# Kernel tuning notes

Hardware: AMD Instinct MI355X
Metric: run time of the kernel (lower is better)

## Reference

```python
import jax, jax.numpy as jnp
import numpy as np

B_IMG, T_PER, DIN = 8, 4096, 1176
D, E, BN, L, TOP_K, OUT = 1024, 8, 64, 4, 2, 4096


def setup_inputs() -> dict:
    key = jax.random.key(0)
    ks = jax.random.split(key, 16)
    s = 0.02
    inp = {
        "pixel_values": jax.random.normal(ks[0], (B_IMG * T_PER, DIN), jnp.float32),
        "image_grid_thw": jnp.tile(jnp.array([[1, 64, 64]], dtype=jnp.int64), (B_IMG, 1)),
        # in_proj (no bias)
        "w_in": jax.random.normal(ks[1], (DIN, D), jnp.float32) * s,
        # skin classifier: Linear(D,64) -> ReLU -> Linear(64,3)
        "w_sc1": jax.random.normal(ks[2], (D, 64), jnp.float32) * s,
        "b_sc1": jnp.zeros((64,), jnp.float32),
        "w_sc2": jax.random.normal(ks[3], (64, 3), jnp.float32) * s,
        "b_sc2": jnp.zeros((3,), jnp.float32),
        # per-adapter-layer routers (stacked over L)
        "w_rimg": jax.random.normal(ks[4], (L, D, E), jnp.float32) * s,
        "w_rskin": jax.random.normal(ks[5], (L, 3, E), jnp.float32) * s,
        # per-layer, per-expert MLP: Linear(D,BN) -> ReLU -> Linear(BN,D)
        "ew1": jax.random.normal(ks[6], (L, E, D, BN), jnp.float32) * s,
        "eb1": jnp.zeros((L, E, BN), jnp.float32),
        "ew2": jax.random.normal(ks[7], (L, E, BN, D), jnp.float32) * s,
        "eb2": jnp.zeros((L, E, D), jnp.float32),
        # out_proj
        "w_out": jax.random.normal(ks[8], (D, OUT), jnp.float32) * s,
        "b_out": jnp.zeros((OUT,), jnp.float32),
    }
    return inp


def _forward(pixel_values, image_grid_thw, w_in, w_sc1, b_sc1, w_sc2, b_sc2,
             w_rimg, w_rskin, ew1, eb1, ew2, eb2, w_out, b_out):
    B = image_grid_thw.shape[0]
    T = pixel_values.shape[0] // B  # equal chunk sizes (t*h*w identical per image)
    x = pixel_values.reshape(B, T, -1)

    def per_image(xc):  # xc: [T, din]
        h = xc @ w_in  # [T, D]
        g = h.mean(0)
        skin_logits = jax.nn.relu(g @ w_sc1 + b_sc1) @ w_sc2 + b_sc2  # [3]
        skin_probs = jax.nn.softmax(skin_logits)

        def layer(carry, params):
            h, aux = carry
            wri, wrs, W1, B1, W2, B2 = params
            logits = h @ wri + skin_probs @ wrs  # [T, E]
            probs = jax.nn.softmax(logits, axis=-1)
            tp, ti = jax.lax.top_k(probs, TOP_K)
            tp = tp / (tp.sum(-1, keepdims=True) + 1e-6)
            rows = jnp.arange(h.shape[0])[:, None]
            # dense per-token expert weights (0 for non-selected experts)
            wfull = jnp.zeros_like(probs).at[rows, ti].add(tp)
            mask = jnp.zeros_like(probs).at[rows, ti].add(1.0)
            h1 = jax.nn.relu(jnp.einsum('td,edb->teb', h, W1) + B1)  # [T,E,BN]
            h2 = jnp.einsum('teb,ebd->ted', h1, W2) + B2             # [T,E,D]
            moe_out = jnp.einsum('ted,te->td', h2, wfull)
            aux = aux + (probs.mean(0) * mask.mean(0)).sum() * probs.shape[-1]
            return (h + moe_out, aux), None

        (h, aux), _ = jax.lax.scan(layer, (h, jnp.zeros((), h.dtype)),
                                   (w_rimg, w_rskin, ew1, eb1, ew2, eb2))
        return h.mean(0), skin_logits, aux

    pooled, skin_logits, aux = jax.vmap(per_image)(x)
    vision_proj = pooled @ w_out + b_out
    return pooled, vision_proj, aux.sum(), skin_logits


def reference(pixel_values, image_grid_thw, w_in, w_sc1, b_sc1, w_sc2, b_sc2,
              w_rimg, w_rskin, ew1, eb1, ew2, eb2, w_out, b_out):
    return _forward(pixel_values, image_grid_thw, w_in, w_sc1, b_sc1, w_sc2, b_sc2,
                    w_rimg, w_rskin, ew1, eb1, ew2, eb2, w_out, b_out)
```

## Files before the change

kernel.cpp:

```cpp
#include <hip/hip_runtime.h>
#include <math.h>

#define TPI  4096
#define TT   32768
#define DIN  1176
#define KP   1184
#define DM   1024
#define NE   8
#define BN   64
#define NL   4
#define DOUT 4096

typedef __attribute__((ext_vector_type(4))) float floatx4;
typedef __attribute__((ext_vector_type(8))) short bf16x8;
typedef unsigned int uint;

__device__ inline short f2bf(float x) {
    unsigned u = __float_as_uint(x);
    u += 0x7fffu + ((u >> 16) & 1u);
    return (short)(u >> 16);
}
__device__ inline float bf2f(short h) {
    return __uint_as_float(((unsigned)(unsigned short)h) << 16);
}

#define GLP(p) ((const __attribute__((address_space(1))) void*)(p))
#define LDSP(p) ((__attribute__((address_space(3))) void*)(p))
#define ASYNC16(g, s) __builtin_amdgcn_global_load_lds(GLP(g), LDSP(s), 16, 0, 0)

#define OFF_H0    0ul
#define OFF_H1    67108864ul
#define OFF_XB    134217728ul
#define OFF_WBT   211812352ul
#define OFF_E1T   214237184ul
#define OFF_E2T   218431488ul
#define OFF_BTOK  222625792ul
#define OFF_BW1   222756864ul
#define OFF_BW2   222887936ul
#define OFF_T2E   223019008ul
#define OFF_T2W   223150080ul
#define OFF_WQ    223412224ul
#define OFF_Z     223416320ul
#define Z_BYTES   38976ul
#define OFF_RB    223455296ul

__global__ __launch_bounds__(256) void convx_kernel(
    const float* __restrict__ X, short* __restrict__ Xb)
{
    const long row = blockIdx.x;
    const float* src = X + row * (long)DIN;
    short* dst = Xb + row * (long)KP;
    for (int i = threadIdx.x; i < 296; i += 256) {
        short4 s;
        if (i < 294) {
            float4 v = *(const float4*)(src + i * 4);
            s.x = f2bf(v.x); s.y = f2bf(v.y); s.z = f2bf(v.z); s.w = f2bf(v.w);
        } else {
            s.x = 0; s.y = 0; s.z = 0; s.w = 0;
        }
        *(short4*)(dst + i * 4) = s;
    }
}

__global__ __launch_bounds__(256) void transp_kernel(
    const float* __restrict__ src, short* __restrict__ dst, int RS, int CS, int DK)
{
    __shared__ float tb[64][65];
    const int kt = blockIdx.x * 64, nt = blockIdx.y * 64;
    const long sb = (long)blockIdx.z * RS * CS;
    const long db = (long)blockIdx.z * CS * DK;
    const int rr = threadIdx.x >> 6, cc = threadIdx.x & 63;
#pragma unroll
    for (int i = 0; i < 16; ++i) {
        int r = i * 4 + rr;
        int k = kt + r, n = nt + cc;
        tb[r][cc] = (k < RS && n < CS) ? src[sb + (long)k * CS + n] : 0.0f;
    }
    __syncthreads();
#pragma unroll
    for (int i = 0; i < 16; ++i) {
        int r = i * 4 + rr;
        int n = nt + r, k = kt + cc;
        if (n < CS && k < DK) dst[db + (long)n * DK + k] = f2bf(tb[cc][r]);
    }
}

__global__ __launch_bounds__(256) void gemm_in_mfma(
    const short* __restrict__ Xb, const short* __restrict__ Wbt, short* __restrict__ Hb)
{
    __shared__ __align__(16) short As[128 * 32];
    __shared__ __align__(16) short Bs[128 * 32];
    const int tid = threadIdx.x;
    const int m0 = blockIdx.x * 128, n0 = blockIdx.y * 128;
    const int w = tid >> 6, lane = tid & 63;
    const int quad = lane >> 4, l15 = lane & 15;
    const int wm = (w >> 1) * 64, wn = (w & 1) * 64;

    floatx4 acc[4][4];
#pragma unroll
    for (int i = 0; i < 4; ++i)
#pragma unroll
        for (int j = 0; j < 4; ++j) acc[i][j] = 0.0f;

    const int r0 = tid >> 2, kof = (tid & 3) * 8;
    const int r1 = (tid + 256) >> 2;
    const short* a0p = Xb + (long)(m0 + r0) * KP + kof;
    const short* a1p = Xb + (long)(m0 + r1) * KP + kof;
    const short* b0p = Wbt + (long)(n0 + r0) * KP + kof;
    const short* b1p = Wbt + (long)(n0 + r1) * KP + kof;
    short* as0 = As + tid * 8;
    short* as1 = As + (tid + 256) * 8;
    short* bs0 = Bs + tid * 8;
    short* bs1 = Bs + (tid + 256) * 8;

    for (int k0 = 0; k0 < KP; k0 += 32) {
        __syncthreads();
        ASYNC16(a0p + k0, as0);
        ASYNC16(a1p + k0, as1);
        ASYNC16(b0p + k0, bs0);
        ASYNC16(b1p + k0, bs1);
        __syncthreads();
        bf16x8 af[4], bfr[4];
#pragma unroll
        for (int i = 0; i < 4; ++i)
            af[i] = *(const bf16x8*)&As[(wm + i * 16 + l15) * 32 + quad * 8];
#pragma unroll
        for (int j = 0; j < 4; ++j)
            bfr[j] = *(const bf16x8*)&Bs[(wn + j * 16 + l15) * 32 + quad * 8];
#pragma unroll
        for (int i = 0; i < 4; ++i)
#pragma unroll
            for (int j = 0; j < 4; ++j)
                acc[i][j] = __builtin_amdgcn_mfma_f32_16x16x32_bf16(af[i], bfr[j], acc[i][j], 0, 0, 0);
    }
#pragma unroll
    for (int i = 0; i < 4; ++i)
#pragma unroll
        for (int j = 0; j < 4; ++j)
#pragma unroll
            for (int r = 0; r < 4; ++r)
                Hb[(long)(m0 + wm + i * 16 + quad * 4 + r) * DM + n0 + wn + j * 16 + l15] =
                    f2bf(acc[i][j][r]);
}

__global__ __launch_bounds__(256) void colmean_kernel(
    const short* __restrict__ Hb, float* __restrict__ outp)
{
    const int col = blockIdx.x * 256 + threadIdx.x;
    const int img = blockIdx.y;
    const int t0 = blockIdx.z * 256;
    const short* p = Hb + ((long)img * TPI + t0) * DM + col;
    float s = 0.0f;
#pragma unroll 8
    for (int t = 0; t < 256; ++t) s += bf2f(p[(long)t * DM]);
    atomicAdd(&outp[img * DM + col], s * (1.0f / 4096.0f));
}

__global__ __launch_bounds__(256) void skin1_kernel(
    const float* __restrict__ g, const float* __restrict__ w_sc1,
    const float* __restrict__ b_sc1, float* __restrict__ hsg)
{
    __shared__ float red[4][64];
    const int img = blockIdx.x;
    const int part = threadIdx.x >> 6, c = threadIdx.x & 63;
    float s = 0.0f;
    for (int i = 0; i < 256; ++i) {
        int d = part * 256 + i;
        s += g[img * DM + d] * w_sc1[d * 64 + c];
    }
    red[part][c] = s;
    __syncthreads();
    if (part == 0) {
        float v = red[0][c] + red[1][c] + red[2][c] + red[3][c] + b_sc1[c];
        hsg[img * 64 + c] = fmaxf(v, 0.0f);
    }
}

__global__ __launch_bounds__(256) void skin2_kernel(
    const float* __restrict__ hsg, const float* __restrict__ w_sc2, const float* __restrict__ b_sc2,
    const float* __restrict__ w_rskin, float* __restrict__ skin_logits_out, float* __restrict__ rb)
{
    __shared__ float l3[24];
    __shared__ float sp[24];
    const int tid = threadIdx.x;
    if (tid < 24) {
        int img = tid / 3, j = tid % 3;
        float s = b_sc2[j];
        for (int c = 0; c < 64; ++c) s += hsg[img * 64 + c] * w_sc2[c * 3 + j];
        l3[tid] = s;
        skin_logits_out[tid] = s;
    }
    __syncthreads();
    if (tid < 8) {
        float v0 = l3[tid * 3], v1 = l3[tid * 3 + 1], v2 = l3[tid * 3 + 2];
        float m = fmaxf(v0, fmaxf(v1, v2));
        float e0 = expf(v0 - m), e1 = expf(v1 - m), e2 = expf(v2 - m);
        float inv = 1.0f / (e0 + e1 + e2);
        sp[tid * 3] = e0 * inv; sp[tid * 3 + 1] = e1 * inv; sp[tid * 3 + 2] = e2 * inv;
    }
    __syncthreads();
    {
        int l = tid >> 6, img = (tid >> 3) & 7, e = tid & 7;
        float s = 0.0f;
#pragma unroll
        for (int c = 0; c < 3; ++c) s += sp[img * 3 + c] * w_rskin[(l * 3 + c) * 8 + e];
        rb[tid] = s;
    }
}

__global__ __launch_bounds__(256) void router_kernel(
    const short* __restrict__ Hb, const float* __restrict__ w_rimg, const float* __restrict__ rb,
    uint* __restrict__ top2e, float* __restrict__ top2w, int* __restrict__ counts_pair,
    float* __restrict__ sum_probs, float* __restrict__ mask_cnt, int l)
{
    __shared__ float wl[DM * NE];
    __shared__ __align__(16) short hs[64 * 64];
    __shared__ float lgS[64 * 8];
    const int tid = threadIdx.x;
    const int tok0 = blockIdx.x * 64;
    const int img = tok0 >> 12;

    const float* wr = w_rimg + (long)l * DM * NE;
#pragma unroll
    for (int i = 0; i < 32; ++i) wl[tid + 256 * i] = wr[tid + 256 * i];

    const int tok = tid & 63, ep = tid >> 6, e0 = ep * 2;
    const int c0 = tid, c1 = tid + 256;
    const short* g0 = Hb + (long)(tok0 + (c0 >> 3)) * DM + (c0 & 7) * 8;
    const short* g1 = Hb + (long)(tok0 + (c1 >> 3)) * DM + (c1 & 7) * 8;
    short* s0 = hs + c0 * 8;
    short* s1 = hs + c1 * 8;

    float a0 = 0.0f, a1 = 0.0f;
    for (int ds = 0; ds < 16; ++ds) {
        __syncthreads();
        ASYNC16(g0 + ds * 64, s0);
        ASYNC16(g1 + ds * 64, s1);
        __syncthreads();
#pragma unroll
        for (int d8 = 0; d8 < 8; ++d8) {
            bf16x8 h8 = *(const bf16x8*)&hs[tok * 64 + d8 * 8];
#pragma unroll
            for (int jj = 0; jj < 8; ++jj) {
                float hv = bf2f(h8[jj]);
                int gd = ds * 64 + d8 * 8 + jj;
                a0 += hv * wl[gd * 8 + e0];
                a1 += hv * wl[gd * 8 + e0 + 1];
            }
        }
    }
    lgS[tok * 8 + e0] = a0;
    lgS[tok * 8 + e0 + 1] = a1;
    __syncthreads();

    if (tid < 64) {
        const int token = tok0 + tid;
        float p[8];
        float mx = -1e30f;
#pragma unroll
        for (int e = 0; e < 8; ++e) {
            float v = lgS[tid * 8 + e] + rb[l * 64 + img * 8 + e];
            p[e] = v; mx = fmaxf(mx, v);
        }
        float s = 0.0f;
#pragma unroll
        for (int e = 0; e < 8; ++e) { p[e] = expf(p[e] - mx); s += p[e]; }
        float inv = 1.0f / s;
#pragma unroll
        for (int e = 0; e < 8; ++e) p[e] *= inv;

        int i1 = 0; float b1v = p[0];
#pragma unroll
        for (int e = 1; e < 8; ++e) if (p[e] > b1v) { b1v = p[e]; i1 = e; }
        int i2 = -1; float b2v = -1.0f;
#pragma unroll
        for (int e = 0; e < 8; ++e) if (e != i1 && p[e] > b2v) { b2v = p[e]; i2 = e; }
        float den = b1v + b2v + 1e-6f;
        top2e[token] = (uint)i1 | ((uint)i2 << 8);
        top2w[2 * token] = b1v / den;
        top2w[2 * token + 1] = b2v / den;

        atomicAdd(&counts_pair[l * 64 + i1 * 8 + i2], 1);

        for (int slot = 0; slot < 2; ++slot) {
            int esel = slot ? i2 : i1;
#pragma unroll
            for (int e = 0; e < 8; ++e) {
                unsigned long long m = __ballot(esel == e);
                int pc = __popcll(m);
                if (pc && tid == (__ffsll(m) - 1))
                    atomicAdd(&mask_cnt[l * 64 + img * 8 + e], (float)pc);
            }
        }
#pragma unroll
        for (int e = 0; e < 8; ++e) {
            float r = p[e];
            for (int off = 32; off > 0; off >>= 1) r += __shfl_down(r, off);
            if (tid == 0) atomicAdd(&sum_probs[l * 64 + img * 8 + e], r);
        }
    }
}

__global__ __launch_bounds__(256) void scatter_kernel(
    const uint* __restrict__ top2e, const float* __restrict__ top2w,
    const int* __restrict__ counts_pair, int* __restrict__ cursors,
    int* __restrict__ btok, float* __restrict__ bw1, float* __restrict__ bw2, int l)
{
    const int t = blockIdx.x * 256 + threadIdx.x;
    const int lane = threadIdx.x & 63;
    uint pe = top2e[t];
    int p = (int)(pe & 255u) * 8 + (int)((pe >> 8) & 255u);
    float w1 = top2w[2 * t], w2 = top2w[2 * t + 1];
    int myoff = 0;
    for (int q = 0; q < 64; ++q) {
        int c = counts_pair[l * 64 + q];
        if (q < p) myoff += c;
    }
    unsigned long long rem = __ballot(true);
    while (rem) {
        int leader = __ffsll(rem) - 1;
        int pv = __shfl(p, leader);
        unsigned long long m = __ballot(p == pv);
        int basep = 0;
        if (lane == leader) basep = atomicAdd(&cursors[l * 64 + pv], __popcll(m));
        basep = __shfl(basep, leader);
        if (p == pv) {
            int pos = basep + __popcll(m & ((1ull << lane) - 1ull));
            int s = myoff + pos;
            btok[s] = t;
            bw1[s] = w1;
            bw2[s] = w2;
        }
        rem &= ~m;
    }
}

__global__ __launch_bounds__(64) void wq_kernel(
    const int* __restrict__ counts_pair, int* __restrict__ wq, int* __restrict__ nworkp, int l)
{
    const int p = threadIdx.x;
    int cnt = counts_pair[l * 64 + p];
    int nb = (cnt + 63) >> 6;
    int x = nb;
    for (int off = 1; off < 64; off <<= 1) {
        int y = __shfl_up(x, off);
        if (p >= off) x += y;
    }
    int start = x - nb;
    for (int i = 0; i < nb; ++i) wq[start + i] = p | ((i * 64) << 6);
    if (p == 63) nworkp[0] = x;
}

__global__ __launch_bounds__(256) void expert_pair(
    const short* __restrict__ Hin, short* __restrict__ Hout,
    const int* __restrict__ counts_pair, const int* __restrict__ btok,
    const float* __restrict__ bw1, const float* __restrict__ bw2,
    const short* __restrict__ ew1t, const float* __restrict__ eb1,
    const short* __restrict__ ew2t, const float* __restrict__ eb2,
    const int* __restrict__ wq, const int* __restrict__ nworkp, int l)
{
    __shared__ __align__(16) short As[64 * 32];
    __shared__ __align__(16) short h1a[64 * 72];
    __shared__ __align__(16) short h1b[64 * 72];
    __shared__ int tkS[64];
    __shared__ float w1S[64], w2S[64];

    const int tid = threadIdx.x;
    const int w = tid >> 6, lane = tid & 63;
    const int quad = lane >> 4, l15 = lane & 15;
    const int nwork = nworkp[0];

    for (int wi = blockIdx.x; wi < nwork; wi += gridDim.x) {
        const int item = wq[wi];
        const int p = item & 63, base = item >> 6;
        const int ea = p >> 3, eb = p & 7;
        int off = 0, cnt = 0;
        for (int q = 0; q < 64; ++q) {
            int c = counts_pair[l * 64 + q];
            if (q < p) off += c;
            if (q == p) cnt = c;
        }
        __syncthreads();
        if (tid < 64) {
            bool valid = (base + tid) < cnt;
            int s = off + base + tid;
            tkS[tid] = valid ? btok[s] : 0;
            w1S[tid] = valid ? bw1[s] : 0.0f;
            w2S[tid] = valid ? bw2[s] : 0.0f;
        }
        __syncthreads();
        const int lea = l * 8 + ea, leb = l * 8 + eb;

        floatx4 acc1a[4], acc1b[4];
#pragma unroll
        for (int i = 0; i < 4; ++i) { acc1a[i] = 0.0f; acc1b[i] = 0.0f; }

        const short* ap = Hin + (long)tkS[tid >> 2] * DM + (tid & 3) * 8;
        const short* w1ap = ew1t + ((long)lea * 64 + w * 16 + l15) * DM + quad * 8;
        const short* w1bp = ew1t + ((long)leb * 64 + w * 16 + l15) * DM + quad * 8;
        short* asd = As + tid * 8;

        for (int k0 = 0; k0 < DM; k0 += 32) {
            __syncthreads();
            ASYNC16(ap + k0, asd);
            __syncthreads();
            bf16x8 ba = *(const bf16x8*)(w1ap + k0);
            bf16x8 bb = *(const bf16x8*)(w1bp + k0);
#pragma unroll
            for (int i = 0; i < 4; ++i) {
                bf16x8 af = *(const bf16x8*)&As[(i * 16 + l15) * 32 + quad * 8];
                acc1a[i] = __builtin_amdgcn_mfma_f32_16x16x32_bf16(af, ba, acc1a[i], 0, 0, 0);
                acc1b[i] = __builtin_amdgcn_mfma_f32_16x16x32_bf16(af, bb, acc1b[i], 0, 0, 0);
            }
        }
        {
            float b1av = eb1[lea * BN + w * 16 + l15];
            float b1bv = eb1[leb * BN + w * 16 + l15];
#pragma unroll
            for (int i = 0; i < 4; ++i)
#pragma unroll
                for (int r = 0; r < 4; ++r) {
                    h1a[(i * 16 + quad * 4 + r) * 72 + w * 16 + l15] =
                        f2bf(fmaxf(acc1a[i][r] + b1av, 0.0f));
                    h1b[(i * 16 + quad * 4 + r) * 72 + w * 16 + l15] =
                        f2bf(fmaxf(acc1b[i][r] + b1bv, 0.0f));
                }
        }
        __syncthreads();

        const short* w2ap = ew2t + ((long)lea * DM + w * 16 + l15) * 64 + quad * 8;
        const short* w2bp = ew2t + ((long)leb * DM + w * 16 + l15) * 64 + quad * 8;
        for (int n0 = 0; n0 < DM; n0 += 64) {
            floatx4 a2a[4], a2b[4];
#pragma unroll
            for (int tj = 0; tj < 4; ++tj) { a2a[tj] = 0.0f; a2b[tj] = 0.0f; }
#pragma unroll
            for (int kk = 0; kk < 2; ++kk) {
                bf16x8 wa = *(const bf16x8*)(w2ap + (long)n0 * 64 + kk * 32);
                bf16x8 wb = *(const bf16x8*)(w2bp + (long)n0 * 64 + kk * 32);
#pragma unroll
                for (int tj = 0; tj < 4; ++tj) {
                    bf16x8 ha = *(const bf16x8*)&h1a[(tj * 16 + l15) * 72 + kk * 32 + quad * 8];
                    bf16x8 hb = *(const bf16x8*)&h1b[(tj * 16 + l15) * 72 + kk * 32 + quad * 8];
                    a2a[tj] = __builtin_amdgcn_mfma_f32_16x16x32_bf16(wa, ha, a2a[tj], 0, 0, 0);
                    a2b[tj] = __builtin_amdgcn_mfma_f32_16x16x32_bf16(wb, hb, a2b[tj], 0, 0, 0);
                }
            }
            const int nb = n0 + w * 16 + quad * 4;
            float4 b2av = *(const float4*)&eb2[lea * DM + nb];
            float4 b2bv = *(const float4*)&eb2[leb * DM + nb];
#pragma unroll
            for (int tj = 0; tj < 4; ++tj) {
                int tk = tj * 16 + l15;
                if (base + tk < cnt) {
                    int t = tkS[tk];
                    float w1 = w1S[tk], w2 = w2S[tk];
                    short4 hres = *(const short4*)&Hin[(long)t * DM + nb];
                    short4 o;
                    o.x = f2bf(bf2f(hres.x) + w1 * (a2a[tj][0] + b2av.x) + w2 * (a2b[tj][0] + b2bv.x));
                    o.y = f2bf(bf2f(hres.y) + w1 * (a2a[tj][1] + b2av.y) + w2 * (a2b[tj][1] + b2bv.y));
                    o.z = f2bf(bf2f(hres.z) + w1 * (a2a[tj][2] + b2av.z) + w2 * (a2b[tj][2] + b2bv.z));
                    o.w = f2bf(bf2f(hres.w) + w1 * (a2a[tj][3] + b2av.w) + w2 * (a2b[tj][3] + b2bv.w));
                    *(short4*)&Hout[(long)t * DM + nb] = o;
                }
            }
        }
    }
}

__global__ __launch_bounds__(256) void vproj_kernel(
    const float* __restrict__ pooled, const float* __restrict__ w_out,
    const float* __restrict__ b_out, float* __restrict__ outp)
{
    __shared__ float ps[8 * 128];
    const int tid = threadIdx.x;
    const int n = blockIdx.x * 256 + tid;
    const int d0 = blockIdx.y * 128;
#pragma unroll
    for (int i = 0; i < 4; ++i) {
        int idx = tid + i * 256;
        ps[idx] = pooled[(idx >> 7) * DM + d0 + (idx & 127)];
    }
    __syncthreads();
    float acc[8];
    float binit = (blockIdx.y == 0) ? b_out[n] : 0.0f;
#pragma unroll
    for (int img = 0; img < 8; ++img) acc[img] = binit;
    for (int d = 0; d < 128; ++d) {
        float wv = w_out[(long)(d0 + d) * DOUT + n];
#pragma unroll
        for (int img = 0; img < 8; ++img) acc[img] += ps[img * 128 + d] * wv;
    }
#pragma unroll
    for (int img = 0; img < 8; ++img) atomicAdd(&outp[img * DOUT + n], acc[img]);
}

__global__ __launch_bounds__(64) void aux_kernel(
    const float* __restrict__ sum_probs, const float* __restrict__ mask_cnt,
    float* __restrict__ outp)
{
    const int tid = threadIdx.x;
    float v = 0.0f;
    if (tid < 32) {
        float s = 0.0f;
#pragma unroll
        for (int e = 0; e < 8; ++e) s += sum_probs[tid * 8 + e] * mask_cnt[tid * 8 + e];
        v = s * (8.0f / (4096.0f * 4096.0f));
    }
    for (int off = 32; off > 0; off >>= 1) v += __shfl_down(v, off);
    if (tid == 0) outp[0] = v;
}

extern "C" void kernel_launch(void* const* d_in, const int* in_sizes, int n_in,
                              void* d_out, int out_size, void* d_ws, size_t ws_size,
                              hipStream_t stream) {
    const float* X       = (const float*)d_in[0];
    const float* w_in    = (const float*)d_in[2];
    const float* w_sc1   = (const float*)d_in[3];
    const float* b_sc1   = (const float*)d_in[4];
    const float* w_sc2   = (const float*)d_in[5];
    const float* b_sc2   = (const float*)d_in[6];
    const float* w_rimg  = (const float*)d_in[7];
    const float* w_rskin = (const float*)d_in[8];
    const float* ew1     = (const float*)d_in[9];
    const float* eb1     = (const float*)d_in[10];
    const float* ew2     = (const float*)d_in[11];
    const float* eb2     = (const float*)d_in[12];
    const float* w_out   = (const float*)d_in[13];
    const float* b_out   = (const float*)d_in[14];

    float* out = (float*)d_out;
    char* ws = (char*)d_ws;

    short* H0   = (short*)(ws + OFF_H0);
    short* H1   = (short*)(ws + OFF_H1);
    short* Xb   = (short*)(ws + OFF_XB);
    short* Wbt  = (short*)(ws + OFF_WBT);
    short* ew1t = (short*)(ws + OFF_E1T);
    short* ew2t = (short*)(ws + OFF_E2T);
    int*   btok = (int*)(ws + OFF_BTOK);
    float* bw1  = (float*)(ws + OFF_BW1);
    float* bw2  = (float*)(ws + OFF_BW2);
    uint*  top2e = (uint*)(ws + OFF_T2E);
    float* top2w = (float*)(ws + OFF_T2W);
    int*   wq    = (int*)(ws + OFF_WQ);
    int*   counts_pair = (int*)(ws + OFF_Z);
    int*   cursors     = (int*)(ws + OFF_Z + 1024);
    int*   nworkp      = (int*)(ws + OFF_Z + 2048);
    float* sum_probs   = (float*)(ws + OFF_Z + 2112);
    float* mask_cnt    = (float*)(ws + OFF_Z + 3136);
    float* g           = (float*)(ws + OFF_Z + 4160);
    float* hsg         = (float*)(ws + OFF_Z + 36928);
    float* rb          = (float*)(ws + OFF_RB);

    hipMemsetAsync(d_out, 0, (size_t)out_size * sizeof(float), stream);
    hipMemsetAsync(ws + OFF_Z, 0, Z_BYTES, stream);

    dim3 b256(256);
    convx_kernel<<<TT, b256, 0, stream>>>(X, Xb);
    transp_kernel<<<dim3(19, 16, 1), b256, 0, stream>>>(w_in, Wbt, DIN, DM, KP);
    transp_kernel<<<dim3(16, 1, 32), b256, 0, stream>>>(ew1, ew1t, DM, BN, DM);
    transp_kernel<<<dim3(1, 16, 32), b256, 0, stream>>>(ew2, ew2t, BN, DM, BN);
    gemm_in_mfma<<<dim3(256, 8), b256, 0, stream>>>(Xb, Wbt, H0);
    colmean_kernel<<<dim3(4, 8, 16), b256, 0, stream>>>(H0, g);
    skin1_kernel<<<8, b256, 0, stream>>>(g, w_sc1, b_sc1, hsg);
    skin2_kernel<<<1, b256, 0, stream>>>(hsg, w_sc2, b_sc2, w_rskin, out + 40961, rb);

    short* Hc = H0;
    short* Hn = H1;
    for (int l = 0; l < NL; ++l) {
        router_kernel<<<512, b256, 0, stream>>>(Hc, w_rimg, rb, top2e, top2w,
                                                counts_pair, sum_probs, mask_cnt, l);
        scatter_kernel<<<128, b256, 0, stream>>>(top2e, top2w, counts_pair, cursors,
                                                 btok, bw1, bw2, l);
        wq_kernel<<<1, 64, 0, stream>>>(counts_pair, wq, nworkp, l);
        expert_pair<<<640, b256, 0, stream>>>(Hc, Hn, counts_pair, btok, bw1, bw2,
                                              ew1t, eb1, ew2t, eb2, wq, nworkp, l);
        short* tmp = Hc; Hc = Hn; Hn = tmp;
    }
    colmean_kernel<<<dim3(4, 8, 16), b256, 0, stream>>>(Hc, out);
    vproj_kernel<<<dim3(16, 8), b256, 0, stream>>>(out, w_out, b_out, out + 8192);
    aux_kernel<<<1, 64, 0, stream>>>(sum_probs, mask_cnt, out + 40960);
}
```

Measured before the change: 1.691 ms.

## Use MFMA router, stage residual rows in LDS, precompute pair offsets

```diff
diff --git a/kernel.cpp b/kernel.cpp
--- a/kernel.cpp
+++ b/kernel.cpp
@@ -41,8 +41,9 @@
 #define OFF_T2W   223150080ul
 #define OFF_WQ    223412224ul
 #define OFF_Z     223416320ul
-#define Z_BYTES   38976ul
-#define OFF_RB    223455296ul
+#define Z_BYTES   39232ul
+#define OFF_RB    223455552ul
+#define OFF_WRT   223456576ul
 
 __global__ __launch_bounds__(256) void convx_kernel(
     const float* __restrict__ X, short* __restrict__ Xb)
@@ -85,6 +86,19 @@
     }
 }
 
+__global__ __launch_bounds__(256) void wrt_kernel(
+    const float* __restrict__ w_rimg, short* __restrict__ wrT)
+{
+    const int l = blockIdx.x >> 4, e = blockIdx.x & 15;
+    short* dst = wrT + ((long)l * 16 + e) * 1024;
+    if (e < 8) {
+        const float* src = w_rimg + (long)l * 8192 + e;
+        for (int k = threadIdx.x; k < 1024; k += 256) dst[k] = f2bf(src[k * 8]);
+    } else {
+        for (int k = threadIdx.x; k < 1024; k += 256) dst[k] = 0;
+    }
+}
+
 __global__ __launch_bounds__(256) void gemm_in_mfma(
     const short* __restrict__ Xb, const short* __restrict__ Wbt, short* __restrict__ Hb)
 {
@@ -209,48 +223,39 @@
 }
 
 __global__ __launch_bounds__(256) void router_kernel(
-    const short* __restrict__ Hb, const float* __restrict__ w_rimg, const float* __restrict__ rb,
+    const short* __restrict__ Hb, const short* __restrict__ wrT, const float* __restrict__ rb,
     uint* __restrict__ top2e, float* __restrict__ top2w, int* __restrict__ counts_pair,
     float* __restrict__ sum_probs, float* __restrict__ mask_cnt, int l)
 {
-    __shared__ float wl[DM * NE];
-    __shared__ __align__(16) short hs[64 * 64];
-    __shared__ float lgS[64 * 8];
+    __shared__ __align__(16) short As[8 * 64 * 32];
+    __shared__ float lgS[64 * 9];
     const int tid = threadIdx.x;
     const int tok0 = blockIdx.x * 64;
     const int img = tok0 >> 12;
-
-    const float* wr = w_rimg + (long)l * DM * NE;
-#pragma unroll
-    for (int i = 0; i < 32; ++i) wl[tid + 256 * i] = wr[tid + 256 * i];
-
-    const int tok = tid & 63, ep = tid >> 6, e0 = ep * 2;
-    const int c0 = tid, c1 = tid + 256;
-    const short* g0 = Hb + (long)(tok0 + (c0 >> 3)) * DM + (c0 & 7) * 8;
-    const short* g1 = Hb + (long)(tok0 + (c1 >> 3)) * DM + (c1 & 7) * 8;
-    short* s0 = hs + c0 * 8;
-    short* s1 = hs + c1 * 8;
-
-    float a0 = 0.0f, a1 = 0.0f;
-    for (int ds = 0; ds < 16; ++ds) {
+    const int w = tid >> 6, lane = tid & 63;
+    const int quad = lane >> 4, l15 = lane & 15;
+
+    const short* rowptr = Hb + (long)(tok0 + w * 16 + (lane >> 2)) * DM + (lane & 3) * 8;
+    short* sdst = As + tid * 8;
+    const short* wrl = wrT + (long)l * 16 * 1024 + l15 * 1024 + quad * 8;
+
+    floatx4 acc = 0.0f;
+    for (int k0 = 0; k0 < DM; k0 += 256) {
         __syncthreads();
-        ASYNC16(g0 + ds * 64, s0);
-        ASYNC16(g1 + ds * 64, s1);
+#pragma unroll
+        for (int c = 0; c < 8; ++c) ASYNC16(rowptr + k0 + c * 32, sdst + c * 2048);
         __syncthreads();
 #pragma unroll
-        for (int d8 = 0; d8 < 8; ++d8) {
-            bf16x8 h8 = *(const bf16x8*)&hs[tok * 64 + d8 * 8];
-#pragma unroll
-            for (int jj = 0; jj < 8; ++jj) {
-                float hv = bf2f(h8[jj]);
-                int gd = ds * 64 + d8 * 8 + jj;
-                a0 += hv * wl[gd * 8 + e0];
-                a1 += hv * wl[gd * 8 + e0 + 1];
-            }
-        }
-    }
-    lgS[tok * 8 + e0] = a0;
-    lgS[tok * 8 + e0 + 1] = a1;
+        for (int c = 0; c < 8; ++c) {
+            bf16x8 af = *(const bf16x8*)&As[c * 2048 + (w * 16 + l15) * 32 + quad * 8];
+            bf16x8 bf = *(const bf16x8*)(wrl + k0 + c * 32);
+            acc = __builtin_amdgcn_mfma_f32_16x16x32_bf16(af, bf, acc, 0, 0, 0);
+        }
+    }
+    if (l15 < 8) {
+#pragma unroll
+        for (int r = 0; r < 4; ++r) lgS[(w * 16 + quad * 4 + r) * 9 + l15] = acc[r];
+    }
     __syncthreads();
 
     if (tid < 64) {
@@ -259,7 +264,7 @@
         float mx = -1e30f;
 #pragma unroll
         for (int e = 0; e < 8; ++e) {
-            float v = lgS[tid * 8 + e] + rb[l * 64 + img * 8 + e];
+            float v = lgS[tid * 9 + e] + rb[l * 64 + img * 8 + e];
             p[e] = v; mx = fmaxf(mx, v);
         }
         float s = 0.0f;
@@ -301,9 +306,32 @@
     }
 }
 
+__global__ __launch_bounds__(64) void wq_kernel(
+    const int* __restrict__ counts_pair, int* __restrict__ wq, int* __restrict__ nworkp,
+    int* __restrict__ pair_off, int l)
+{
+    const int p = threadIdx.x;
+    int cnt = counts_pair[l * 64 + p];
+    int x = cnt;
+    for (int off = 1; off < 64; off <<= 1) {
+        int y = __shfl_up(x, off);
+        if (p >= off) x += y;
+    }
+    pair_off[p] = x - cnt;
+    int nb = (cnt + 63) >> 6;
+    int t = nb;
+    for (int off = 1; off < 64; off <<= 1) {
+        int y = __shfl_up(t, off);
+        if (p >= off) t += y;
+    }
+    int start = t - nb;
+    for (int i = 0; i < nb; ++i) wq[start + i] = p | ((i * 64) << 6);
+    if (p == 63) nworkp[0] = t;
+}
+
 __global__ __launch_bounds__(256) void scatter_kernel(
     const uint* __restrict__ top2e, const float* __restrict__ top2w,
-    const int* __restrict__ counts_pair, int* __restrict__ cursors,
+    const int* __restrict__ pair_off, int* __restrict__ cursors,
     int* __restrict__ btok, float* __restrict__ bw1, float* __restrict__ bw2, int l)
 {
     const int t = blockIdx.x * 256 + threadIdx.x;
@@ -311,11 +339,7 @@
     uint pe = top2e[t];
     int p = (int)(pe & 255u) * 8 + (int)((pe >> 8) & 255u);
     float w1 = top2w[2 * t], w2 = top2w[2 * t + 1];
-    int myoff = 0;
-    for (int q = 0; q < 64; ++q) {
-        int c = counts_pair[l * 64 + q];
-        if (q < p) myoff += c;
-    }
+    int myoff = pair_off[p];
     unsigned long long rem = __ballot(true);
     while (rem) {
         int leader = __ffsll(rem) - 1;
@@ -335,31 +359,15 @@
     }
 }
 
-__global__ __launch_bounds__(64) void wq_kernel(
-    const int* __restrict__ counts_pair, int* __restrict__ wq, int* __restrict__ nworkp, int l)
-{
-    const int p = threadIdx.x;
-    int cnt = counts_pair[l * 64 + p];
-    int nb = (cnt + 63) >> 6;
-    int x = nb;
-    for (int off = 1; off < 64; off <<= 1) {
-        int y = __shfl_up(x, off);
-        if (p >= off) x += y;
-    }
-    int start = x - nb;
-    for (int i = 0; i < nb; ++i) wq[start + i] = p | ((i * 64) << 6);
-    if (p == 63) nworkp[0] = x;
-}
-
 __global__ __launch_bounds__(256) void expert_pair(
     const short* __restrict__ Hin, short* __restrict__ Hout,
-    const int* __restrict__ counts_pair, const int* __restrict__ btok,
-    const float* __restrict__ bw1, const float* __restrict__ bw2,
+    const int* __restrict__ counts_pair, const int* __restrict__ pair_off,
+    const int* __restrict__ btok, const float* __restrict__ bw1, const float* __restrict__ bw2,
     const short* __restrict__ ew1t, const float* __restrict__ eb1,
     const short* __restrict__ ew2t, const float* __restrict__ eb2,
     const int* __restrict__ wq, const int* __restrict__ nworkp, int l)
 {
-    __shared__ __align__(16) short As[64 * 32];
+    __shared__ __align__(16) short As[8 * 64 * 32];
     __shared__ __align__(16) short h1a[64 * 72];
     __shared__ __align__(16) short h1b[64 * 72];
     __shared__ int tkS[64];
@@ -369,17 +377,15 @@
     const int w = tid >> 6, lane = tid & 63;
     const int quad = lane >> 4, l15 = lane & 15;
     const int nwork = nworkp[0];
+    short* sdst = As + tid * 8;
 
     for (int wi = blockIdx.x; wi < nwork; wi += gridDim.x) {
         const int item = wq[wi];
         const int p = item & 63, base = item >> 6;
         const int ea = p >> 3, eb = p & 7;
-        int off = 0, cnt = 0;
-        for (int q = 0; q < 64; ++q) {
-            int c = counts_pair[l * 64 + q];
-            if (q < p) off += c;
-            if (q == p) cnt = c;
-        }
+        const int off = pair_off[p];
+        const int cnt = counts_pair[l * 64 + p];
+
         __syncthreads();
         if (tid < 64) {
             bool valid = (base + tid) < cnt;
@@ -390,27 +396,29 @@
         }
         __syncthreads();
         const int lea = l * 8 + ea, leb = l * 8 + eb;
+        const short* rowptr = Hin + (long)tkS[w * 16 + (lane >> 2)] * DM + (lane & 3) * 8;
 
         floatx4 acc1a[4], acc1b[4];
 #pragma unroll
         for (int i = 0; i < 4; ++i) { acc1a[i] = 0.0f; acc1b[i] = 0.0f; }
-
-        const short* ap = Hin + (long)tkS[tid >> 2] * DM + (tid & 3) * 8;
         const short* w1ap = ew1t + ((long)lea * 64 + w * 16 + l15) * DM + quad * 8;
         const short* w1bp = ew1t + ((long)leb * 64 + w * 16 + l15) * DM + quad * 8;
-        short* asd = As + tid * 8;
-
-        for (int k0 = 0; k0 < DM; k0 += 32) {
+
+        for (int k0 = 0; k0 < DM; k0 += 256) {
             __syncthreads();
-            ASYNC16(ap + k0, asd);
+#pragma unroll
+            for (int c = 0; c < 8; ++c) ASYNC16(rowptr + k0 + c * 32, sdst + c * 2048);
             __syncthreads();
-            bf16x8 ba = *(const bf16x8*)(w1ap + k0);
-            bf16x8 bb = *(const bf16x8*)(w1bp + k0);
-#pragma unroll
-            for (int i = 0; i < 4; ++i) {
-                bf16x8 af = *(const bf16x8*)&As[(i * 16 + l15) * 32 + quad * 8];
-                acc1a[i] = __builtin_amdgcn_mfma_f32_16x16x32_bf16(af, ba, acc1a[i], 0, 0, 0);
-                acc1b[i] = __builtin_amdgcn_mfma_f32_16x16x32_bf16(af, bb, acc1b[i], 0, 0, 0);
+#pragma unroll
+            for (int c = 0; c < 8; ++c) {
+                bf16x8 ba = *(const bf16x8*)(w1ap + k0 + c * 32);
+                bf16x8 bb = *(const bf16x8*)(w1bp + k0 + c * 32);
+#pragma unroll
+                for (int i = 0; i < 4; ++i) {
+                    bf16x8 af = *(const bf16x8*)&As[c * 2048 + (i * 16 + l15) * 32 + quad * 8];
+                    acc1a[i] = __builtin_amdgcn_mfma_f32_16x16x32_bf16(af, ba, acc1a[i], 0, 0, 0);
+                    acc1b[i] = __builtin_amdgcn_mfma_f32_16x16x32_bf16(af, bb, acc1b[i], 0, 0, 0);
+                }
             }
         }
         {
@@ -430,40 +438,64 @@
 
         const short* w2ap = ew2t + ((long)lea * DM + w * 16 + l15) * 64 + quad * 8;
         const short* w2bp = ew2t + ((long)leb * DM + w * 16 + l15) * 64 + quad * 8;
-        for (int n0 = 0; n0 < DM; n0 += 64) {
-            floatx4 a2a[4], a2b[4];
-#pragma unroll
-            for (int tj = 0; tj < 4; ++tj) { a2a[tj] = 0.0f; a2b[tj] = 0.0f; }
-#pragma unroll
-            for (int kk = 0; kk < 2; ++kk) {
-                bf16x8 wa = *(const bf16x8*)(w2ap + (long)n0 * 64 + kk * 32);
-                bf16x8 wb = *(const bf16x8*)(w2bp + (long)n0 * 64 + kk * 32);
+        const bool rowvalid = (base + (tid >> 2)) < cnt;
+        const long orow = (long)tkS[tid >> 2] * DM;
+
+        for (int gidx = 0; gidx < 4; ++gidx) {
+            const int g0 = gidx * 256;
+#pragma unroll
+            for (int c = 0; c < 8; ++c) ASYNC16(rowptr + g0 + c * 32, sdst + c * 2048);
+            __syncthreads();
+#pragma unroll
+            for (int ns = 0; ns < 4; ++ns) {
+                const int n0 = g0 + ns * 64;
+                floatx4 a2a[4], a2b[4];
+#pragma unroll
+                for (int tj = 0; tj < 4; ++tj) { a2a[tj] = 0.0f; a2b[tj] = 0.0f; }
+#pragma unroll
+                for (int kk = 0; kk < 2; ++kk) {
+                    bf16x8 wa = *(const bf16x8*)(w2ap + (long)n0 * 64 + kk * 32);
+                    bf16x8 wb = *(const bf16x8*)(w2bp + (long)n0 * 64 + kk * 32);
+#pragma unroll
+                    for (int tj = 0; tj < 4; ++tj) {
+                        bf16x8 ha = *(const bf16x8*)&h1a[(tj * 16 + l15) * 72 + kk * 32 + quad * 8];
+                        bf16x8 hb = *(const bf16x8*)&h1b[(tj * 16 + l15) * 72 + kk * 32 + quad * 8];
+                        a2a[tj] = __builtin_amdgcn_mfma_f32_16x16x32_bf16(wa, ha, a2a[tj], 0, 0, 0);
+                        a2b[tj] = __builtin_amdgcn_mfma_f32_16x16x32_bf16(wb, hb, a2b[tj], 0, 0, 0);
+                    }
+                }
+                const int nloc = ns * 64 + w * 16 + quad * 4;
+                const int csub = nloc >> 5, cidx = nloc & 31;
+                float4 b2av = *(const float4*)&eb2[lea * DM + g0 + nloc];
+                float4 b2bv = *(const float4*)&eb2[leb * DM + g0 + nloc];
 #pragma unroll
                 for (int tj = 0; tj < 4; ++tj) {
-                    bf16x8 ha = *(const bf16x8*)&h1a[(tj * 16 + l15) * 72 + kk * 32 + quad * 8];
-                    bf16x8 hb = *(const bf16x8*)&h1b[(tj * 16 + l15) * 72 + kk * 32 + quad * 8];
-                    a2a[tj] = __builtin_amdgcn_mfma_f32_16x16x32_bf16(wa, ha, a2a[tj], 0, 0, 0);
-                    a2b[tj] = __builtin_amdgcn_mfma_f32_16x16x32_bf16(wb, hb, a2b[tj], 0, 0, 0);
+                    int tk = tj * 16 + l15;
+                    float w1 = w1S[tk], w2 = w2S[tk];
+                    short* slot = &As[csub * 2048 + tk * 32 + cidx];
+                    short4 res = *(short4*)slot;
+                    short4 o;
+                    o.x = f2bf(bf2f(res.x) + w1 * (a2a[tj][0] + b2av.x) + w2 * (a2b[tj][0] + b2bv.x));
+                    o.y = f2bf(bf2f(res.y) + w1 * (a2a[tj][1] + b2av.y) + w2 * (a2b[tj][1] + b2bv.y));
+                    o.z = f2bf(bf2f(res.z) + w1 * (a2a[tj][2] + b2av.z) + w2 * (a2b[tj][2] + b2bv.z));
+                    o.w = f2bf(bf2f(res.w) + w1 * (a2a[tj][3] + b2av.w) + w2 * (a2b[tj][3] + b2bv.w));
+                    *(short4*)slot = o;
                 }
             }
-            const int nb = n0 + w * 16 + quad * 4;
-            float4 b2av = *(const float4*)&eb2[lea * DM + nb];
-            float4 b2bv = *(const float4*)&eb2[leb * DM + nb];
-#pragma unroll
-            for (int tj = 0; tj < 4; ++tj) {
-                int tk = tj * 16 + l15;
-                if (base + tk < cnt) {
-                    int t = tkS[tk];
-                    float w1 = w1S[tk], w2 = w2S[tk];
-                    short4 hres = *(const short4*)&Hin[(long)t * DM + nb];
-                    short4 o;
-                    o.x = f2bf(bf2f(hres.x) + w1 * (a2a[tj][0] + b2av.x) + w2 * (a2b[tj][0] + b2bv.x));
-                    o.y = f2bf(bf2f(hres.y) + w1 * (a2a[tj][1] + b2av.y) + w2 * (a2b[tj][1] + b2bv.y));
-                    o.z = f2bf(bf2f(hres.z) + w1 * (a2a[tj][2] + b2av.z) + w2 * (a2b[tj][2] + b2bv.z));
-                    o.w = f2bf(bf2f(hres.w) + w1 * (a2a[tj][3] + b2av.w) + w2 * (a2b[tj][3] + b2bv.w));
-                    *(short4*)&Hout[(long)t * DM + nb] = o;
+            __syncthreads();
+            if (rowvalid) {
+                const int tok = tid >> 2;
+#pragma unroll
+                for (int c2 = 0; c2 < 2; ++c2) {
+                    const int csub = (tid & 3) * 2 + c2;
+#pragma unroll
+                    for (int j = 0; j < 4; ++j) {
+                        int4 v = *(const int4*)&As[csub * 2048 + tok * 32 + j * 8];
+                        *(int4*)(Hout + orow + g0 + csub * 32 + j * 8) = v;
+                    }
                 }
             }
+            __syncthreads();
         }
     }
 }
@@ -547,11 +579,13 @@
     int*   counts_pair = (int*)(ws + OFF_Z);
     int*   cursors     = (int*)(ws + OFF_Z + 1024);
     int*   nworkp      = (int*)(ws + OFF_Z + 2048);
-    float* sum_probs   = (float*)(ws + OFF_Z + 2112);
-    float* mask_cnt    = (float*)(ws + OFF_Z + 3136);
-    float* g           = (float*)(ws + OFF_Z + 4160);
-    float* hsg         = (float*)(ws + OFF_Z + 36928);
+    int*   pair_off    = (int*)(ws + OFF_Z + 2112);
+    float* sum_probs   = (float*)(ws + OFF_Z + 2368);
+    float* mask_cnt    = (float*)(ws + OFF_Z + 3392);
+    float* g           = (float*)(ws + OFF_Z + 4416);
+    float* hsg         = (float*)(ws + OFF_Z + 37184);
     float* rb          = (float*)(ws + OFF_RB);
+    short* wrT         = (short*)(ws + OFF_WRT);
 
     hipMemsetAsync(d_out, 0, (size_t)out_size * sizeof(float), stream);
     hipMemsetAsync(ws + OFF_Z, 0, Z_BYTES, stream);
@@ -561,6 +595,7 @@
     transp_kernel<<<dim3(19, 16, 1), b256, 0, stream>>>(w_in, Wbt, DIN, DM, KP);
     transp_kernel<<<dim3(16, 1, 32), b256, 0, stream>>>(ew1, ew1t, DM, BN, DM);
     transp_kernel<<<dim3(1, 16, 32), b256, 0, stream>>>(ew2, ew2t, BN, DM, BN);
+    wrt_kernel<<<64, b256, 0, stream>>>(w_rimg, wrT);
     gemm_in_mfma<<<dim3(256, 8), b256, 0, stream>>>(Xb, Wbt, H0);
     colmean_kernel<<<dim3(4, 8, 16), b256, 0, stream>>>(H0, g);
     skin1_kernel<<<8, b256, 0, stream>>>(g, w_sc1, b_sc1, hsg);
@@ -569,12 +604,12 @@
     short* Hc = H0;
     short* Hn = H1;
     for (int l = 0; l < NL; ++l) {
-        router_kernel<<<512, b256, 0, stream>>>(Hc, w_rimg, rb, top2e, top2w,
+        router_kernel<<<512, b256, 0, stream>>>(Hc, wrT, rb, top2e, top2w,
                                                 counts_pair, sum_probs, mask_cnt, l);
-        scatter_kernel<<<128, b256, 0, stream>>>(top2e, top2w, counts_pair, cursors,
+        wq_kernel<<<1, 64, 0, stream>>>(counts_pair, wq, nworkp, pair_off, l);
+        scatter_kernel<<<128, b256, 0, stream>>>(top2e, top2w, pair_off, cursors,
                                                  btok, bw1, bw2, l);
-        wq_kernel<<<1, 64, 0, stream>>>(counts_pair, wq, nworkp, l);
-        expert_pair<<<640, b256, 0, stream>>>(Hc, Hn, counts_pair, btok, bw1, bw2,
+        expert_pair<<<576, b256, 0, stream>>>(Hc, Hn, counts_pair, pair_off, btok, bw1, bw2,
                                               ew1t, eb1, ew2t, eb2, wq, nworkp, l);
         short* tmp = Hc; Hc = Hn; Hn = tmp;
     }
```

After: 1.493 ms. 11.7% less time.
